# Optimization experiments

Measured on AMD Instinct MI355X. Metric: run time of the kernel, lower is better.

The kernel has to match this reference:

```python
import jax, jax.numpy as jnp
import numpy as np

HIDDEN = 2048
NUM_HEADS = 16
NUM_KV_HEADS = 16
QK_NOPE = 128
QK_ROPE = 64
HEAD_DIM = QK_NOPE + QK_ROPE  # 192
V_HEAD = 128
KV_LORA = 512
Q_LORA = 1536
EPS = 1e-6


def rmsnorm(x, w):
    var = jnp.mean(x * x, axis=-1, keepdims=True)
    return x * jax.lax.rsqrt(var + EPS) * w


def setup_inputs() -> dict:
    key = jax.random.key(0)
    ks = jax.random.split(key, 8)
    s = lambda fan_in: 1.0 / np.sqrt(fan_in)
    return {
        "hidden_states": jax.random.normal(ks[0], (2, 2048, HIDDEN), jnp.float32),
        # weights stored as [in, out] so forward is x @ W
        "q_a_w": jax.random.normal(ks[1], (HIDDEN, Q_LORA), jnp.float32) * s(HIDDEN),
        "q_a_ln_w": jnp.ones((Q_LORA,), jnp.float32),
        "q_b_w": jax.random.normal(ks[2], (Q_LORA, NUM_HEADS * HEAD_DIM), jnp.float32) * s(Q_LORA),
        "kv_a_w": jax.random.normal(ks[3], (HIDDEN, KV_LORA + NUM_KV_HEADS * QK_ROPE), jnp.float32) * s(HIDDEN),
        "kv_a_ln_w": jnp.ones((KV_LORA,), jnp.float32),
        "kv_b_w": jax.random.normal(ks[4], (KV_LORA, NUM_KV_HEADS * (QK_NOPE + V_HEAD)), jnp.float32) * s(KV_LORA),
        "o_w": jax.random.normal(ks[5], (NUM_HEADS * V_HEAD, HIDDEN), jnp.float32) * s(NUM_HEADS * V_HEAD),
    }


def reference(hidden_states, q_a_w, q_a_ln_w, q_b_w, kv_a_w, kv_a_ln_w, kv_b_w, o_w):
    B, T, _ = hidden_states.shape
    # Q path: low-rank down-proj -> RMSNorm -> up-proj
    q = rmsnorm(hidden_states @ q_a_w, q_a_ln_w) @ q_b_w
    q = q.reshape(B, T, NUM_HEADS, HEAD_DIM)  # [B,T,H,192]

    # KV path: joint down-proj producing latent + rope slice
    kv_raw = hidden_states @ kv_a_w
    kv_latent = rmsnorm(kv_raw[..., :KV_LORA], kv_a_ln_w)
    k_rope = kv_raw[..., KV_LORA:].reshape(B, T, NUM_KV_HEADS, QK_ROPE)
    kv = (kv_latent @ kv_b_w).reshape(B, T, NUM_KV_HEADS, QK_NOPE + V_HEAD)
    k_nope = kv[..., :QK_NOPE]
    v = kv[..., QK_NOPE:]  # [B,T,Hkv,128]

    # NOTE: the original forward computes RoPE cos/sin but never applies the
    # rotation; q_rope/k_rope are used as-is (faithfully reproduced here).
    k = jnp.concatenate([k_nope, k_rope], axis=-1)  # [B,T,Hkv,192]
    # num_kv_groups == 1, so no repeat_interleave needed

    scale = 1.0 / jnp.sqrt(jnp.float32(HEAD_DIM))
    scores = jnp.einsum("bqhd,bkhd->bhqk", q, k) * scale  # [B,H,T,T]
    causal = jnp.tril(jnp.ones((T, T), bool))
    scores = jnp.where(causal, scores, jnp.finfo(scores.dtype).min)
    probs = jax.nn.softmax(scores, axis=-1)
    attn = jnp.einsum("bhqk,bkhd->bqhd", probs, v)  # [B,T,H,128]
    attn = attn.reshape(B, T, NUM_HEADS * V_HEAD)
    return attn @ o_w
```

## Files before the change

kernel.cpp:

```cpp
#include <hip/hip_runtime.h>
#include <cstdint>
#include <cstddef>

typedef unsigned short u16;
typedef short short8 __attribute__((ext_vector_type(8)));
typedef float f32x4 __attribute__((ext_vector_type(4)));

#define B_   2
#define T_   2048
#define H_   16
#define HID_ 2048
#define DQK_ 192
#define DV_  128
#define AW_  3072

__device__ __forceinline__ float bf2f(u16 u) {
  unsigned int v = ((unsigned int)u) << 16;
  return __builtin_bit_cast(float, v);
}
__device__ __forceinline__ u16 f2bf(float f) {
  unsigned int u = __builtin_bit_cast(unsigned int, f);
  u += 0x7fff + ((u >> 16) & 1);
  return (u16)(u >> 16);
}
__device__ __forceinline__ void load_lds16(const void* g, void* l) {
  __builtin_amdgcn_global_load_lds((const __attribute__((address_space(1))) void*)g,
                                   (__attribute__((address_space(3))) void*)l, 16, 0, 0);
}

__global__ __launch_bounds__(256) void cast_f32_bf16(const float* __restrict__ x,
                                                     u16* __restrict__ y) {
  size_t i = ((size_t)blockIdx.x * 256 + threadIdx.x) * 8;
  float4 a = *(const float4*)&x[i];
  float4 b = *(const float4*)&x[i + 4];
  u16 r[8];
  r[0] = f2bf(a.x); r[1] = f2bf(a.y); r[2] = f2bf(a.z); r[3] = f2bf(a.w);
  r[4] = f2bf(b.x); r[5] = f2bf(b.y); r[6] = f2bf(b.z); r[7] = f2bf(b.w);
  *(uint4*)&y[i] = *(const uint4*)&r[0];
}

__global__ __launch_bounds__(256) void transpose_cast_k(const float* __restrict__ W,
                                                        u16* __restrict__ Wt,
                                                        int K, int N) {
  __shared__ u16 tile[32][33];
  int n0 = blockIdx.x * 32, k0 = blockIdx.y * 32;
  int tx = threadIdx.x & 31, ty = threadIdx.x >> 5;
#pragma unroll
  for (int i = 0; i < 32; i += 8)
    tile[ty + i][tx] = f2bf(W[(size_t)(k0 + ty + i) * N + n0 + tx]);
  __syncthreads();
#pragma unroll
  for (int i = 0; i < 32; i += 8)
    Wt[(size_t)(n0 + ty + i) * K + k0 + tx] = tile[tx][ty + i];
}

__global__ __launch_bounds__(256) void rmsnorm_k(const u16* __restrict__ in, int in_stride,
                                                 int L, const float* __restrict__ w,
                                                 u16* __restrict__ out, int out_stride) {
  int row = blockIdx.x;
  const u16* x = in + (size_t)row * in_stride;
  float ss = 0.f;
  for (int i = threadIdx.x * 8; i < L; i += 2048) {
    uint4 v = *(const uint4*)&x[i];
    const u16* p = (const u16*)&v;
#pragma unroll
    for (int e = 0; e < 8; ++e) { float f = bf2f(p[e]); ss += f * f; }
  }
#pragma unroll
  for (int m = 32; m >= 1; m >>= 1) ss += __shfl_xor(ss, m);
  __shared__ float red[4];
  if ((threadIdx.x & 63) == 0) red[threadIdx.x >> 6] = ss;
  __syncthreads();
  ss = red[0] + red[1] + red[2] + red[3];
  float inv = rsqrtf(ss / (float)L + 1e-6f);
  u16* o = out + (size_t)row * out_stride;
  for (int i = threadIdx.x * 8; i < L; i += 2048) {
    uint4 v = *(const uint4*)&x[i];
    const u16* p = (const u16*)&v;
    u16 r8[8];
#pragma unroll
    for (int e = 0; e < 8; ++e) r8[e] = f2bf(bf2f(p[e]) * inv * w[i + e]);
    *(uint4*)&o[i] = *(const uint4*)&r8[0];
  }
}

template <int EPI>
__global__ __launch_bounds__(256) void gemm_bt(const u16* __restrict__ A,
                                               const u16* __restrict__ Bt,
                                               void* __restrict__ Cout,
                                               int M, int N, int K) {
  __shared__ u16 As[3][128 * 32];
  __shared__ u16 Bs[3][128 * 32];
  const int nbx = N >> 7;
  const int bx = blockIdx.x % nbx, by = blockIdx.x / nbx;
  const int m0 = by << 7, n0 = bx << 7;
  const int tid = threadIdx.x, w = tid >> 6, lane = tid & 63;
  const int wr = w >> 1, wc = w & 1;
  const int llo = lane & 15, lhi = lane >> 4;
  f32x4 acc[4][4] = {};

  const int c0 = tid, c1 = tid + 256;
  const int ar0 = c0 >> 2, s0_ = c0 & 3;
  const int ar1 = c1 >> 2, s1_ = c1 & 3;
  const u16* Asrc0 = A + (size_t)(m0 + ar0) * K + (s0_ ^ ((ar0 >> 1) & 3)) * 8;
  const u16* Asrc1 = A + (size_t)(m0 + ar1) * K + (s1_ ^ ((ar1 >> 1) & 3)) * 8;
  const u16* Bsrc0 = Bt + (size_t)(n0 + ar0) * K + (s0_ ^ ((ar0 >> 1) & 3)) * 8;
  const u16* Bsrc1 = Bt + (size_t)(n0 + ar1) * K + (s1_ ^ ((ar1 >> 1) & 3)) * 8;

  int aoff[4], boff[4];
#pragma unroll
  for (int i = 0; i < 4; ++i) {
    int rowa = wr * 64 + i * 16 + llo;
    aoff[i] = (rowa * 4 + (lhi ^ ((rowa >> 1) & 3))) * 8;
    int rowb = wc * 64 + i * 16 + llo;
    boff[i] = (rowb * 4 + (lhi ^ ((rowb >> 1) & 3))) * 8;
  }

#define STAGE_KT(kt, buf)                                   \
  do {                                                      \
    int k0_ = (kt) << 5;                                    \
    load_lds16(Asrc0 + k0_, &As[(buf)][c0 * 8]);            \
    load_lds16(Asrc1 + k0_, &As[(buf)][c1 * 8]);            \
    load_lds16(Bsrc0 + k0_, &Bs[(buf)][c0 * 8]);            \
    load_lds16(Bsrc1 + k0_, &Bs[(buf)][c1 * 8]);            \
  } while (0)

  const int NT = K >> 5;
  STAGE_KT(0, 0);
  STAGE_KT(1, 1);
  asm volatile("s_waitcnt vmcnt(4)" ::: "memory");
  __builtin_amdgcn_s_barrier();

  int cur = 0, nxt = 2;
  for (int kt = 0; kt < NT; ++kt) {
    if (kt + 2 < NT) STAGE_KT(kt + 2, nxt);
    short8 af[4], bfr[4];
#pragma unroll
    for (int i = 0; i < 4; ++i) af[i] = *(const short8*)&As[cur][aoff[i]];
#pragma unroll
    for (int j = 0; j < 4; ++j) bfr[j] = *(const short8*)&Bs[cur][boff[j]];
    __builtin_amdgcn_s_setprio(1);
#pragma unroll
    for (int i = 0; i < 4; ++i)
#pragma unroll
      for (int j = 0; j < 4; ++j)
        acc[i][j] = __builtin_amdgcn_mfma_f32_16x16x32_bf16(af[i], bfr[j], acc[i][j], 0, 0, 0);
    __builtin_amdgcn_s_setprio(0);
    if (kt + 2 < NT) asm volatile("s_waitcnt vmcnt(4)" ::: "memory");
    else             asm volatile("s_waitcnt vmcnt(0)" ::: "memory");
    __builtin_amdgcn_s_barrier();
    cur = (cur == 2) ? 0 : cur + 1;
    nxt = (nxt == 2) ? 0 : nxt + 1;
  }
#undef STAGE_KT

  if constexpr (EPI == 0) {
    float* C = (float*)Cout;
#pragma unroll
    for (int i = 0; i < 4; ++i)
#pragma unroll
      for (int j = 0; j < 4; ++j)
#pragma unroll
        for (int r = 0; r < 4; ++r)
          C[(size_t)(m0 + wr * 64 + i * 16 + lhi * 4 + r) * N + (n0 + wc * 64 + j * 16 + llo)] =
              acc[i][j][r];
  } else {
    const float scale = (EPI == 3) ? 0.10412163f : 1.0f;
    u16* C = (u16*)Cout;
#pragma unroll
    for (int i = 0; i < 4; ++i)
#pragma unroll
      for (int j = 0; j < 4; ++j)
#pragma unroll
        for (int r = 0; r < 4; ++r)
          C[(size_t)(m0 + wr * 64 + i * 16 + lhi * 4 + r) * N + (n0 + wc * 64 + j * 16 + llo)] =
              f2bf(acc[i][j][r] * scale);
  }
}

__global__ __launch_bounds__(256) void pack_vt_k(const u16* __restrict__ kv, u16* __restrict__ Vt) {
  __shared__ u16 tile[64][136];
  const int nt = T_ / 64;
  int t0 = (blockIdx.x % nt) * 64;
  int bh = blockIdx.x / nt;
  int b = bh >> 4, h = bh & 15;
  int row = threadIdx.x >> 4;
  int ck = threadIdx.x & 15;
#pragma unroll
  for (int i = 0; i < 64; i += 16) {
    uint4 v = *(const uint4*)&kv[((size_t)(b * T_) + t0 + row + i) * 4096 + h * 256 + 128 + ck * 8];
    *(uint4*)&tile[row + i][ck * 8] = v;
  }
  __syncthreads();
  int d = threadIdx.x >> 1;
  int th = (threadIdx.x & 1) * 32;
  u16 tmp[32];
#pragma unroll
  for (int e = 0; e < 32; ++e) tmp[e] = tile[th + e][d];
#pragma unroll
  for (int e = 0; e < 32; e += 8)
    *(uint4*)&Vt[((size_t)bh * 128 + d) * T_ + t0 + th + e] = *(const uint4*)&tmp[e];
}

__global__ __launch_bounds__(256, 2) void attn_k(const u16* __restrict__ q,
                                                 const u16* __restrict__ kv,
                                                 const u16* __restrict__ kvraw,
                                                 const u16* __restrict__ Vt,
                                                 u16* __restrict__ att) {
  constexpr int KLD = 192, VLD = 64, PLD = 64;
  __shared__ u16 Ks[2][64 * KLD];
  __shared__ u16 Vs[128 * VLD];
  __shared__ u16 Ps[64 * PLD];
  const int idx = (int)blockIdx.x;
  const int bh = idx >> 4, pr = idx & 15;
  const int b = bh >> 4, h = bh & 15;
  const int bT = b * T_;
  const int tid = threadIdx.x, w = tid >> 6, lane = tid & 63;
  const int llo = lane & 15, lhi = lane >> 4;
  const u16* Vb = Vt + (size_t)bh * DV_ * T_;

  const u16* kbase[6]; int kstr[6];
#pragma unroll
  for (int ii = 0; ii < 6; ++ii) {
    int c = ii * 256 + tid;
    int rr = c / 24, chk = c - rr * 24;
    int sc = chk ^ (rr & 7);
    if (sc < 16) { kbase[ii] = kv + (size_t)(bT + rr) * 4096 + h * 256 + sc * 8; kstr[ii] = 4096; }
    else { kbase[ii] = kvraw + (size_t)(bT + rr) * AW_ + 2048 + h * 64 + (sc - 16) * 8; kstr[ii] = AW_; }
  }
  int voff[4];
#pragma unroll
  for (int ii = 0; ii < 4; ++ii) {
    int c = ii * 256 + tid;
    int rr = c >> 3, chk = c & 7;
    voff[ii] = rr * T_ + (chk ^ (rr & 7)) * 8;
  }

#pragma unroll
  for (int pass = 0; pass < 2; ++pass) {
    const int qt = pass == 0 ? 31 - pr : pr;
    const int q0 = qt * 64;
    const int rbase = q0 + w * 16;
    short8 qf[6];
#pragma unroll
    for (int kk = 0; kk < 6; ++kk)
      qf[kk] = *(const short8*)&q[(size_t)(bT + rbase + llo) * AW_ + h * DQK_ + kk * 32 + lhi * 8];
    f32x4 oacc[8] = {};
    float m_r[4], l_r[4];
#pragma unroll
    for (int r = 0; r < 4; ++r) { m_r[r] = -1e30f; l_r[r] = 0.f; }

#pragma unroll
    for (int ii = 0; ii < 6; ++ii)
      load_lds16(kbase[ii], &Ks[0][(ii * 256 + tid) * 8]);
    asm volatile("s_waitcnt vmcnt(0)" ::: "memory");
    __builtin_amdgcn_s_barrier();
    __builtin_amdgcn_sched_barrier(0);

    const int nkt = qt + 1;
    int cur = 0;
    for (int kt = 0; kt < nkt; ++kt) {
      const int k0 = kt * 64;
      const bool hasNext = (kt + 1 < nkt);
#pragma unroll
      for (int ii = 0; ii < 4; ++ii)
        load_lds16(Vb + k0 + voff[ii], &Vs[(ii * 256 + tid) * 8]);
      if (hasNext) {
        u16* kd = Ks[cur ^ 1];
#pragma unroll
        for (int ii = 0; ii < 6; ++ii)
          load_lds16(kbase[ii] + (size_t)(k0 + 64) * kstr[ii], &kd[(ii * 256 + tid) * 8]);
      }
      const u16* kbuf = Ks[cur];
      f32x4 s[4] = {};
      __builtin_amdgcn_s_setprio(1);
#pragma unroll
      for (int kk = 0; kk < 6; ++kk) {
        const int col = kk * 32 + lhi * 8;
        short8 kf[4];
#pragma unroll
        for (int j = 0; j < 4; ++j) {
          const int row = j * 16 + llo;
          kf[j] = *(const short8*)&kbuf[row * KLD + (col ^ ((row & 7) << 3))];
        }
#pragma unroll
        for (int j = 0; j < 4; ++j)
          s[j] = __builtin_amdgcn_mfma_f32_16x16x32_bf16(qf[kk], kf[j], s[j], 0, 0, 0);
      }
      __builtin_amdgcn_s_setprio(0);
      const bool needMask = (k0 + 63 > rbase);
#pragma unroll
      for (int r = 0; r < 4; ++r) {
        const int qrow = rbase + lhi * 4 + r;
        float sv[4];
#pragma unroll
        for (int j = 0; j < 4; ++j) {
          float x = s[j][r];
          if (needMask) { int kcol = k0 + j * 16 + llo; x = (kcol <= qrow) ? x : -1e30f; }
          sv[j] = x;
        }
        float mx = fmaxf(fmaxf(sv[0], sv[1]), fmaxf(sv[2], sv[3]));
#pragma unroll
        for (int mk = 1; mk < 16; mk <<= 1) mx = fmaxf(mx, __shfl_xor(mx, mk));
        if (!__all(mx - m_r[r] <= 8.f)) {
          float mnew = fmaxf(m_r[r], mx);
          float alpha = exp2f(m_r[r] - mnew);
          m_r[r] = mnew;
          l_r[r] *= alpha;
#pragma unroll
          for (int jo = 0; jo < 8; ++jo) oacc[jo][r] *= alpha;
        }
        float rs = 0.f;
        const int prow = w * 16 + lhi * 4 + r;
#pragma unroll
        for (int j = 0; j < 4; ++j) {
          float p = exp2f(sv[j] - m_r[r]);
          rs += p;
          int pcol = j * 16 + llo;
          Ps[prow * PLD + (pcol ^ ((prow & 7) << 3))] = f2bf(p);
        }
        l_r[r] += rs;
      }
      if (hasNext) asm volatile("s_waitcnt vmcnt(6)" ::: "memory");
      else         asm volatile("s_waitcnt vmcnt(0)" ::: "memory");
      __builtin_amdgcn_s_barrier();
      __builtin_amdgcn_sched_barrier(0);
      __builtin_amdgcn_s_setprio(1);
#pragma unroll
      for (int kk2 = 0; kk2 < 2; ++kk2) {
        const int prow = w * 16 + llo;
        const int pcol = kk2 * 32 + lhi * 8;
        short8 pf = *(const short8*)&Ps[prow * PLD + (pcol ^ ((prow & 7) << 3))];
#pragma unroll
        for (int jo = 0; jo < 8; ++jo) {
          const int vrow = jo * 16 + llo;
          short8 vf = *(const short8*)&Vs[vrow * VLD + (pcol ^ ((vrow & 7) << 3))];
          oacc[jo] = __builtin_amdgcn_mfma_f32_16x16x32_bf16(pf, vf, oacc[jo], 0, 0, 0);
        }
      }
      __builtin_amdgcn_s_setprio(0);
      asm volatile("s_waitcnt vmcnt(0)" ::: "memory");
      __builtin_amdgcn_s_barrier();
      __builtin_amdgcn_sched_barrier(0);
      cur ^= 1;
    }
#pragma unroll
    for (int r = 0; r < 4; ++r) {
      float lr = l_r[r];
#pragma unroll
      for (int mk = 1; mk < 16; mk <<= 1) lr += __shfl_xor(lr, mk);
      const int qrow = rbase + lhi * 4 + r;
      const float linv = 1.f / lr;
#pragma unroll
      for (int jo = 0; jo < 8; ++jo)
        att[((size_t)bT + qrow) * (H_ * DV_) + h * DV_ + jo * 16 + llo] =
            f2bf(oacc[jo][r] * linv);
    }
  }
}

extern "C" void kernel_launch(void* const* d_in, const int* in_sizes, int n_in,
                              void* d_out, int out_size, void* d_ws, size_t ws_size,
                              hipStream_t stream) {
  const float* hs      = (const float*)d_in[0];
  const float* q_a_w   = (const float*)d_in[1];
  const float* q_a_ln  = (const float*)d_in[2];
  const float* q_b_w   = (const float*)d_in[3];
  const float* kv_a_w  = (const float*)d_in[4];
  const float* kv_a_ln = (const float*)d_in[5];
  const float* kv_b_w  = (const float*)d_in[6];
  const float* o_w     = (const float*)d_in[7];
  float* out = (float*)d_out;
  char* ws = (char*)d_ws;

  u16* hid  = (u16*)(ws + 0);
  u16* wt   = (u16*)(ws + 16777216);
  u16* qa   = (u16*)(ws + 29360128);
  u16* qan  = (u16*)(ws + 54525952);
  u16* qout = (u16*)(ws + 67108864);
  u16* att  = (u16*)(ws + 92274688);
  u16* kv   = (u16*)(ws + 109051904);
  u16* Vt   = (u16*)(ws + 142606336);

  cast_f32_bf16<<<4096, 256, 0, stream>>>(hs, hid);

  transpose_cast_k<<<dim3(1536 / 32, 2048 / 32), 256, 0, stream>>>(q_a_w, wt, 2048, 1536);
  transpose_cast_k<<<dim3(1536 / 32, 2048 / 32), 256, 0, stream>>>(kv_a_w, wt + (size_t)1536 * 2048, 2048, 1536);
  gemm_bt<1><<<(3072 / 128) * (4096 / 128), 256, 0, stream>>>(hid, wt, qa, 4096, 3072, 2048);

  rmsnorm_k<<<4096, 256, 0, stream>>>(qa, AW_, 1536, q_a_ln, qan, 1536);

  transpose_cast_k<<<dim3(3072 / 32, 1536 / 32), 256, 0, stream>>>(q_b_w, wt, 1536, 3072);
  gemm_bt<3><<<(3072 / 128) * (4096 / 128), 256, 0, stream>>>(qan, wt, qout, 4096, 3072, 1536);

  rmsnorm_k<<<4096, 256, 0, stream>>>(qa + 1536, AW_, 512, kv_a_ln, qan, 512);

  transpose_cast_k<<<dim3(4096 / 32, 512 / 32), 256, 0, stream>>>(kv_b_w, wt, 512, 4096);
  gemm_bt<1><<<(4096 / 128) * (4096 / 128), 256, 0, stream>>>(qan, wt, kv, 4096, 4096, 512);

  pack_vt_k<<<1024, 256, 0, stream>>>(kv, Vt);

  attn_k<<<512, 256, 0, stream>>>(qout, kv, qa, Vt, att);

  transpose_cast_k<<<dim3(2048 / 32, 2048 / 32), 256, 0, stream>>>(o_w, wt, 2048, 2048);
  gemm_bt<0><<<(2048 / 128) * (4096 / 128), 256, 0, stream>>>(att, wt, out, 4096, 2048, 2048);
}
```

Baseline: 366.0 us.

## Enlarge attention query tile to 128 rows with two subtiles per wave

The attention kernel now gives each block a 128-row query tile, with every wave holding two 16-row query subtiles. Each K/V tile staged in LDS therefore feeds twice as many MFMAs, and the two-pass pairing of light and heavy causal tiles is replaced by a block-index mapping that schedules heavy tiles first. The aim is to halve K/V global and LDS traffic per query row and raise MFMA density. The cost is higher register pressure (the min-2-blocks launch bound is dropped, oacc doubles) and coarser causal load balance, since each block now does uneven work.

Result: slower. 427.0 us (+16.6%).

```diff
diff --git a/kernel.cpp b/kernel.cpp
--- a/kernel.cpp
+++ b/kernel.cpp
@@ -202,21 +202,25 @@
     *(uint4*)&Vt[((size_t)bh * 128 + d) * T_ + t0 + th + e] = *(const uint4*)&tmp[e];
 }
 
-__global__ __launch_bounds__(256, 2) void attn_k(const u16* __restrict__ q,
-                                                 const u16* __restrict__ kv,
-                                                 const u16* __restrict__ kvraw,
-                                                 const u16* __restrict__ Vt,
-                                                 u16* __restrict__ att) {
+__global__ __launch_bounds__(256) void attn_k(const u16* __restrict__ q,
+                                              const u16* __restrict__ kv,
+                                              const u16* __restrict__ kvraw,
+                                              const u16* __restrict__ Vt,
+                                              u16* __restrict__ att) {
   constexpr int KLD = 192, VLD = 64, PLD = 64;
   __shared__ u16 Ks[2][64 * KLD];
   __shared__ u16 Vs[128 * VLD];
-  __shared__ u16 Ps[64 * PLD];
+  __shared__ u16 Ps[128 * PLD];
   const int idx = (int)blockIdx.x;
-  const int bh = idx >> 4, pr = idx & 15;
+  int bh, qt;
+  if (idx < 256) { bh = idx & 31; qt = 15 - (idx >> 5); }
+  else           { bh = idx & 31; qt = (idx - 256) >> 5; }
   const int b = bh >> 4, h = bh & 15;
   const int bT = b * T_;
+  const int q0 = qt * 128;
   const int tid = threadIdx.x, w = tid >> 6, lane = tid & 63;
   const int llo = lane & 15, lhi = lane >> 4;
+  const int rbase = q0 + w * 32;
   const u16* Vb = Vt + (size_t)bh * DV_ * T_;
 
   const u16* kbase[6]; int kstr[6];
@@ -236,127 +240,137 @@
     voff[ii] = rr * T_ + (chk ^ (rr & 7)) * 8;
   }
 
-#pragma unroll
-  for (int pass = 0; pass < 2; ++pass) {
-    const int qt = pass == 0 ? 31 - pr : pr;
-    const int q0 = qt * 64;
-    const int rbase = q0 + w * 16;
-    short8 qf[6];
+  short8 qf[2][6];
+#pragma unroll
+  for (int i = 0; i < 2; ++i)
 #pragma unroll
     for (int kk = 0; kk < 6; ++kk)
-      qf[kk] = *(const short8*)&q[(size_t)(bT + rbase + llo) * AW_ + h * DQK_ + kk * 32 + lhi * 8];
-    f32x4 oacc[8] = {};
-    float m_r[4], l_r[4];
-#pragma unroll
-    for (int r = 0; r < 4; ++r) { m_r[r] = -1e30f; l_r[r] = 0.f; }
-
-#pragma unroll
-    for (int ii = 0; ii < 6; ++ii)
-      load_lds16(kbase[ii], &Ks[0][(ii * 256 + tid) * 8]);
-    asm volatile("s_waitcnt vmcnt(0)" ::: "memory");
-    __builtin_amdgcn_s_barrier();
-    __builtin_amdgcn_sched_barrier(0);
-
-    const int nkt = qt + 1;
-    int cur = 0;
-    for (int kt = 0; kt < nkt; ++kt) {
-      const int k0 = kt * 64;
-      const bool hasNext = (kt + 1 < nkt);
-#pragma unroll
-      for (int ii = 0; ii < 4; ++ii)
-        load_lds16(Vb + k0 + voff[ii], &Vs[(ii * 256 + tid) * 8]);
-      if (hasNext) {
-        u16* kd = Ks[cur ^ 1];
-#pragma unroll
-        for (int ii = 0; ii < 6; ++ii)
-          load_lds16(kbase[ii] + (size_t)(k0 + 64) * kstr[ii], &kd[(ii * 256 + tid) * 8]);
+      qf[i][kk] = *(const short8*)&q[(size_t)(bT + rbase + i * 16 + llo) * AW_ + h * DQK_ + kk * 32 + lhi * 8];
+  f32x4 oacc[2][8] = {};
+  float m_r[2][4], l_r[2][4];
+#pragma unroll
+  for (int i = 0; i < 2; ++i)
+#pragma unroll
+    for (int r = 0; r < 4; ++r) { m_r[i][r] = -1e30f; l_r[i][r] = 0.f; }
+
+#pragma unroll
+  for (int ii = 0; ii < 6; ++ii)
+    load_lds16(kbase[ii], &Ks[0][(ii * 256 + tid) * 8]);
+  asm volatile("s_waitcnt vmcnt(0)" ::: "memory");
+  __builtin_amdgcn_s_barrier();
+  __builtin_amdgcn_sched_barrier(0);
+
+  const int nkt = 2 * qt + 2;
+  int cur = 0;
+  for (int kt = 0; kt < nkt; ++kt) {
+    const int k0 = kt * 64;
+    const bool hasNext = (kt + 1 < nkt);
+#pragma unroll
+    for (int ii = 0; ii < 4; ++ii)
+      load_lds16(Vb + k0 + voff[ii], &Vs[(ii * 256 + tid) * 8]);
+    if (hasNext) {
+      u16* kd = Ks[cur ^ 1];
+#pragma unroll
+      for (int ii = 0; ii < 6; ++ii)
+        load_lds16(kbase[ii] + (size_t)(k0 + 64) * kstr[ii], &kd[(ii * 256 + tid) * 8]);
+    }
+    const u16* kbuf = Ks[cur];
+    f32x4 s[2][4] = {};
+    __builtin_amdgcn_s_setprio(1);
+#pragma unroll
+    for (int kk = 0; kk < 6; ++kk) {
+      const int col = kk * 32 + lhi * 8;
+      short8 kf[4];
+#pragma unroll
+      for (int j = 0; j < 4; ++j) {
+        const int row = j * 16 + llo;
+        kf[j] = *(const short8*)&kbuf[row * KLD + (col ^ ((row & 7) << 3))];
       }
-      const u16* kbuf = Ks[cur];
-      f32x4 s[4] = {};
-      __builtin_amdgcn_s_setprio(1);
-#pragma unroll
-      for (int kk = 0; kk < 6; ++kk) {
-        const int col = kk * 32 + lhi * 8;
-        short8 kf[4];
+#pragma unroll
+      for (int i = 0; i < 2; ++i)
+#pragma unroll
+        for (int j = 0; j < 4; ++j)
+          s[i][j] = __builtin_amdgcn_mfma_f32_16x16x32_bf16(qf[i][kk], kf[j], s[i][j], 0, 0, 0);
+    }
+    __builtin_amdgcn_s_setprio(0);
+    const bool needMask = (k0 + 63 > rbase);
+#pragma unroll
+    for (int i = 0; i < 2; ++i)
+#pragma unroll
+      for (int r = 0; r < 4; ++r) {
+        const int qrow = rbase + i * 16 + lhi * 4 + r;
+        float sv[4];
 #pragma unroll
         for (int j = 0; j < 4; ++j) {
-          const int row = j * 16 + llo;
-          kf[j] = *(const short8*)&kbuf[row * KLD + (col ^ ((row & 7) << 3))];
-        }
-#pragma unroll
-        for (int j = 0; j < 4; ++j)
-          s[j] = __builtin_amdgcn_mfma_f32_16x16x32_bf16(qf[kk], kf[j], s[j], 0, 0, 0);
-      }
-      __builtin_amdgcn_s_setprio(0);
-      const bool needMask = (k0 + 63 > rbase);
-#pragma unroll
-      for (int r = 0; r < 4; ++r) {
-        const int qrow = rbase + lhi * 4 + r;
-        float sv[4];
-#pragma unroll
-        for (int j = 0; j < 4; ++j) {
-          float x = s[j][r];
+          float x = s[i][j][r];
           if (needMask) { int kcol = k0 + j * 16 + llo; x = (kcol <= qrow) ? x : -1e30f; }
           sv[j] = x;
         }
         float mx = fmaxf(fmaxf(sv[0], sv[1]), fmaxf(sv[2], sv[3]));
 #pragma unroll
         for (int mk = 1; mk < 16; mk <<= 1) mx = fmaxf(mx, __shfl_xor(mx, mk));
-        if (!__all(mx - m_r[r] <= 8.f)) {
-          float mnew = fmaxf(m_r[r], mx);
-          float alpha = exp2f(m_r[r] - mnew);
-          m_r[r] = mnew;
-          l_r[r] *= alpha;
-#pragma unroll
-          for (int jo = 0; jo < 8; ++jo) oacc[jo][r] *= alpha;
+        if (!__all(mx - m_r[i][r] <= 8.f)) {
+          float mnew = fmaxf(m_r[i][r], mx);
+          float alpha = exp2f(m_r[i][r] - mnew);
+          m_r[i][r] = mnew;
+          l_r[i][r] *= alpha;
+#pragma unroll
+          for (int jo = 0; jo < 8; ++jo) oacc[i][jo][r] *= alpha;
         }
         float rs = 0.f;
-        const int prow = w * 16 + lhi * 4 + r;
+        const int prow = w * 32 + i * 16 + lhi * 4 + r;
 #pragma unroll
         for (int j = 0; j < 4; ++j) {
-          float p = exp2f(sv[j] - m_r[r]);
+          float p = exp2f(sv[j] - m_r[i][r]);
           rs += p;
           int pcol = j * 16 + llo;
           Ps[prow * PLD + (pcol ^ ((prow & 7) << 3))] = f2bf(p);
         }
-        l_r[r] += rs;
+        l_r[i][r] += rs;
       }
-      if (hasNext) asm volatile("s_waitcnt vmcnt(6)" ::: "memory");
-      else         asm volatile("s_waitcnt vmcnt(0)" ::: "memory");
-      __builtin_amdgcn_s_barrier();
-      __builtin_amdgcn_sched_barrier(0);
-      __builtin_amdgcn_s_setprio(1);
-#pragma unroll
-      for (int kk2 = 0; kk2 < 2; ++kk2) {
-        const int prow = w * 16 + llo;
-        const int pcol = kk2 * 32 + lhi * 8;
-        short8 pf = *(const short8*)&Ps[prow * PLD + (pcol ^ ((prow & 7) << 3))];
-#pragma unroll
-        for (int jo = 0; jo < 8; ++jo) {
-          const int vrow = jo * 16 + llo;
-          short8 vf = *(const short8*)&Vs[vrow * VLD + (pcol ^ ((vrow & 7) << 3))];
-          oacc[jo] = __builtin_amdgcn_mfma_f32_16x16x32_bf16(pf, vf, oacc[jo], 0, 0, 0);
-        }
+    if (hasNext) asm volatile("s_waitcnt vmcnt(6)" ::: "memory");
+    else         asm volatile("s_waitcnt vmcnt(0)" ::: "memory");
+    __builtin_amdgcn_s_barrier();
+    __builtin_amdgcn_sched_barrier(0);
+    __builtin_amdgcn_s_setprio(1);
+#pragma unroll
+    for (int kk2 = 0; kk2 < 2; ++kk2) {
+      const int pcol = kk2 * 32 + lhi * 8;
+      short8 pf[2];
+#pragma unroll
+      for (int i = 0; i < 2; ++i) {
+        const int prow = w * 32 + i * 16 + llo;
+        pf[i] = *(const short8*)&Ps[prow * PLD + (pcol ^ ((prow & 7) << 3))];
       }
-      __builtin_amdgcn_s_setprio(0);
-      asm volatile("s_waitcnt vmcnt(0)" ::: "memory");
-      __builtin_amdgcn_s_barrier();
-      __builtin_amdgcn_sched_barrier(0);
-      cur ^= 1;
+#pragma unroll
+      for (int jo = 0; jo < 8; ++jo) {
+        const int vrow = jo * 16 + llo;
+        short8 vf = *(const short8*)&Vs[vrow * VLD + (pcol ^ ((vrow & 7) << 3))];
+#pragma unroll
+        for (int i = 0; i < 2; ++i)
+          oacc[i][jo] = __builtin_amdgcn_mfma_f32_16x16x32_bf16(pf[i], vf, oacc[i][jo], 0, 0, 0);
+      }
     }
+    __builtin_amdgcn_s_setprio(0);
+    asm volatile("s_waitcnt vmcnt(0)" ::: "memory");
+    __builtin_amdgcn_s_barrier();
+    __builtin_amdgcn_sched_barrier(0);
+    cur ^= 1;
+  }
+#pragma unroll
+  for (int i = 0; i < 2; ++i)
 #pragma unroll
     for (int r = 0; r < 4; ++r) {
-      float lr = l_r[r];
+      float lr = l_r[i][r];
 #pragma unroll
       for (int mk = 1; mk < 16; mk <<= 1) lr += __shfl_xor(lr, mk);
-      const int qrow = rbase + lhi * 4 + r;
+      const int qrow = rbase + i * 16 + lhi * 4 + r;
       const float linv = 1.f / lr;
 #pragma unroll
       for (int jo = 0; jo < 8; ++jo)
         att[((size_t)bT + qrow) * (H_ * DV_) + h * DV_ + jo * 16 + llo] =
-            f2bf(oacc[jo][r] * linv);
+            f2bf(oacc[i][jo][r] * linv);
     }
-  }
 }
 
 extern "C" void kernel_launch(void* const* d_in, const int* in_sizes, int n_in,
```
